# Kernel tuning notes

Hardware: AMD Instinct MI355X
Metric: run time of the kernel (lower is better)

The kernel has to match this reference:

```python
import jax, jax.numpy as jnp
import numpy as np

EMB = 256
HEADS = 16
QKV = 16
SQRT_EMB = 16.0
SQRT_QKV = 4.0
CLIP = 10.0


def setup_inputs() -> dict:
    key = jax.random.key(0)
    ks = jax.random.split(key, 8)
    B, M, J = 64, 128, 512
    s = 1.0 / np.sqrt(EMB)
    return {
        "encoded_machine": jax.random.normal(ks[0], (B, M, EMB), jnp.float32),
        "encoded_jobs": jax.random.normal(ks[1], (B, J, EMB), jnp.float32),
        "ninf_mask": jnp.zeros((B, M, J + 1), jnp.float32),
        "Wq3": jax.random.normal(ks[2], (EMB, HEADS * QKV), jnp.float32) * s,
        "Wk": jax.random.normal(ks[3], (EMB, HEADS * QKV), jnp.float32) * s,
        "Wv": jax.random.normal(ks[4], (EMB, HEADS * QKV), jnp.float32) * s,
        "Wc": jax.random.normal(ks[5], (HEADS * QKV, EMB), jnp.float32) * s,
        "bc": jax.random.normal(ks[6], (EMB,), jnp.float32) * s,
        "skip_emb": jax.random.uniform(ks[7], (1, 1, EMB), jnp.float32),
    }


def _heads(x):
    # (B, N, H*D) -> (B, H, N, D)
    B, N, _ = x.shape
    return x.reshape(B, N, HEADS, QKV).transpose(0, 2, 1, 3)


def reference(encoded_machine, encoded_jobs, ninf_mask, Wq3, Wk, Wv, Wc, bc, skip_emb):
    B, M, _ = encoded_machine.shape
    # prepend learned skip token: (B, T=J+1, E)
    jobs = jnp.concatenate(
        [jnp.broadcast_to(skip_emb, (B, 1, EMB)), encoded_jobs], axis=1)
    T = jobs.shape[1]

    q = _heads(encoded_machine @ Wq3)          # (B,H,M,D)
    k = _heads(jobs @ Wk)                      # (B,H,T,D)
    v = _heads(jobs @ Wv)                      # (B,H,T,D)

    score = jnp.einsum("bhmd,bhtd->bhmt", q, k) / SQRT_QKV
    weights = jax.nn.softmax(score, axis=-1)   # (B,H,M,T)
    out = jnp.einsum("bhmt,bhtd->bhmd", weights, v)
    out_concat = out.transpose(0, 2, 1, 3).reshape(B, M, HEADS * QKV)
    mh = out_concat @ Wc + bc                  # (B,M,E)

    score2 = jnp.einsum("bme,bte->bmt", mh, jobs) / SQRT_EMB
    logits = CLIP * jnp.tanh(score2) + ninf_mask
    probs = jax.nn.softmax(logits.reshape(B, M * T), axis=1)
    return probs
```

## Files before the change

### kernel.cpp

```cpp
#include <hip/hip_runtime.h>
#include <math.h>


#define LDT 68
#define LDB 132
#define TPAD 544
#define NROWS 34816

typedef __attribute__((ext_vector_type(8))) short bf16x8;
typedef __attribute__((ext_vector_type(8))) unsigned short u16x8;
typedef __attribute__((ext_vector_type(4))) float f32x4;
typedef __attribute__((ext_vector_type(4))) unsigned short u16x4;

static __device__ inline unsigned short f2bf(float x) {
  unsigned u = __float_as_uint(x);
  return (unsigned short)((u + 0x7fffu + ((u >> 16) & 1u)) >> 16);
}
static __device__ inline float bf2f(unsigned short h) {
  return __uint_as_float(((unsigned)h) << 16);
}

#define GLD16(gsrc, ldst) \
  __builtin_amdgcn_global_load_lds((const __attribute__((address_space(1))) void*)(gsrc), \
                                   (__attribute__((address_space(3))) void*)(ldst), 16, 0, 0)

__global__ void prep_wt(const float* __restrict__ Wk, const float* __restrict__ Wv,
                        unsigned short* __restrict__ Wh, unsigned short* __restrict__ Wl)
{
  __shared__ unsigned short sh[256], sl[256];
  const int c = blockIdx.x, k = threadIdx.x;
  const float x = (c < 256) ? Wk[k * 256 + c] : Wv[k * 256 + (c - 256)];
  const unsigned short h = f2bf(x);
  sh[k] = h; sl[k] = f2bf(x - bf2f(h));
  __syncthreads();
  if (k < 32)
    *(u16x8*)(Wh + ((size_t)k * 512 + c) * 8) = *(const u16x8*)&sh[k * 8];
  else if (k < 64)
    *(u16x8*)(Wl + ((size_t)(k - 32) * 512 + c) * 8) = *(const u16x8*)&sl[(k - 32) * 8];
}

__global__ __launch_bounds__(256) void prep_jobs(
    const float* __restrict__ jobs, const float* __restrict__ skip,
    unsigned short* __restrict__ Jh, unsigned short* __restrict__ Jl)
{
  const int w = threadIdx.x >> 6, lane = threadIdx.x & 63;
  const int r = blockIdx.x * 64 + lane;
  const int bb = r / TPAD, tt = r - bb * TPAD;
  const bool padr = (tt >= 513);
  const float* src = (tt == 0) ? skip : (jobs + ((size_t)(bb * 512 + tt - 1) << 8));
  #pragma unroll
  for (int i = 0; i < 8; ++i) {
    const int cc = w * 8 + i;
    u16x8 h8 = {}, l8 = {};
    if (!padr) {
      const float4 a = *(const float4*)(src + cc * 8);
      const float4 b = *(const float4*)(src + cc * 8 + 4);
      const float v[8] = {a.x,a.y,a.z,a.w, b.x,b.y,b.z,b.w};
      #pragma unroll
      for (int j = 0; j < 8; ++j) {
        const unsigned short hh = f2bf(v[j]);
        h8[j] = hh;
        l8[j] = f2bf(v[j] - bf2f(hh));
      }
    }
    const size_t o = ((size_t)cc * NROWS + r) * 8;
    *(u16x8*)(Jh + o) = h8;
    *(u16x8*)(Jl + o) = l8;
  }
}

__global__ __launch_bounds__(256) void gemm_kv_mfma(
    const unsigned short* __restrict__ Jh, const unsigned short* __restrict__ Jl,
    const unsigned short* __restrict__ Wh, const unsigned short* __restrict__ Wl,
    unsigned short* __restrict__ Kh, unsigned short* __restrict__ Kl,
    unsigned short* __restrict__ Vth, unsigned short* __restrict__ Vtl)
{
  __shared__ __align__(128) char smem[49152];
  const int tid = threadIdx.x;
  const int lin = blockIdx.x + (blockIdx.y << 2);
  const int virt = (lin & 7) * 272 + (lin >> 3);
  const int bx = virt & 3, by = virt >> 2;
  const int w = __builtin_amdgcn_readfirstlane(tid >> 6);
  const int lane = tid & 63;
  const int wr = (w >> 1) << 5;
  const int wc = (w & 1) << 6;
  const int fm = lane & 15, fq = lane >> 4;

  const unsigned short* sp = (w == 0) ? Jh : (w == 1) ? Jl : (w == 2) ? Wh : Wl;
  const char* srcb = (w < 2)
      ? (const char*)sp + ((size_t)(by * 64) + lane) * 16
      : (const char*)sp + ((size_t)(bx * 128) + lane) * 16;

  auto STAGE = [&](int ks, int bsel) {
    char* buf = smem + bsel * 24576;
    if (w < 2) {
      char* dst = buf + (w ? 4096 : 0);
      #pragma unroll
      for (int j = 0; j < 4; ++j)
        GLD16(srcb + ((size_t)(ks * 4 + j)) * ((size_t)NROWS * 16),
              dst + j * 1024);
    } else {
      char* dst = buf + 8192 + ((w == 3) ? 8192 : 0);
      #pragma unroll
      for (int j = 0; j < 8; ++j) {
        const int fq_ = j >> 1, half = j & 1;
        GLD16(srcb + (((size_t)(ks * 4 + fq_)) * 512 + half * 64) * 16,
              dst + fq_ * 2048 + half * 1024);
      }
    }
  };

  f32x4 acc[2][4] = {};

  STAGE(0, 0);
  STAGE(1, 1);

  #pragma unroll
  for (int ks = 0; ks < 8; ++ks) {
    if (ks < 7) {
      if (w < 2) asm volatile("s_waitcnt vmcnt(4)" ::: "memory");
      else       asm volatile("s_waitcnt vmcnt(8)" ::: "memory");
    } else {
      asm volatile("s_waitcnt vmcnt(0)" ::: "memory");
    }
    __builtin_amdgcn_s_barrier();
    __builtin_amdgcn_sched_barrier(0);

    char* cur = smem + (ks & 1) * 24576;
    bf16x8 afh[2], afl[2], bfh[4], bfl[4];
    #pragma unroll
    for (int i = 0; i < 2; ++i) {
      const int ro = fq * 1024 + (wr + i * 16 + fm) * 16;
      afh[i] = *(const bf16x8*)(cur + ro);
      afl[i] = *(const bf16x8*)(cur + 4096 + ro);
    }
    #pragma unroll
    for (int n = 0; n < 4; ++n) {
      const int co = fq * 2048 + (wc + n * 16 + fm) * 16;
      bfh[n] = *(const bf16x8*)(cur + 8192 + co);
      bfl[n] = *(const bf16x8*)(cur + 16384 + co);
    }
    #pragma unroll
    for (int mi = 0; mi < 2; ++mi)
      #pragma unroll
      for (int ni = 0; ni < 4; ++ni) {
        acc[mi][ni] = __builtin_amdgcn_mfma_f32_16x16x32_bf16(afh[mi], bfl[ni], acc[mi][ni], 0, 0, 0);
        acc[mi][ni] = __builtin_amdgcn_mfma_f32_16x16x32_bf16(afl[mi], bfh[ni], acc[mi][ni], 0, 0, 0);
        acc[mi][ni] = __builtin_amdgcn_mfma_f32_16x16x32_bf16(afh[mi], bfh[ni], acc[mi][ni], 0, 0, 0);
      }

    __builtin_amdgcn_s_barrier();
    if (ks + 2 < 8) STAGE(ks + 2, ks & 1);
  }

  const int cb = ((bx & 1) << 7) + wc;
  if (bx < 2) {
    #pragma unroll
    for (int mi = 0; mi < 2; ++mi) {
      #pragma unroll
      for (int r = 0; r < 4; ++r) {
        const int row = by * 64 + wr + mi * 16 + fq * 4 + r;
        const size_t rb = (size_t)row << 8;
        #pragma unroll
        for (int ni = 0; ni < 4; ++ni) {
          const int cc = cb + ni * 16 + fm;
          const float x = acc[mi][ni][r];
          const unsigned short hh = f2bf(x);
          Kh[rb + cc] = hh;
          Kl[rb + cc] = f2bf(x - bf2f(hh));
        }
      }
    }
  } else {
    #pragma unroll
    for (int mi = 0; mi < 2; ++mi) {
      const int row0 = by * 64 + wr + mi * 16 + fq * 4;
      const int bb = row0 / TPAD;
      const int tt0 = row0 - bb * TPAD;
      #pragma unroll
      for (int ni = 0; ni < 4; ++ni) {
        const int cc = cb + ni * 16 + fm;
        const size_t vb = ((size_t)(bb * 256 + cc)) * TPAD + tt0;
        u16x4 vh, vl;
        #pragma unroll
        for (int r = 0; r < 4; ++r) {
          const float x = acc[mi][ni][r];
          const unsigned short hh = f2bf(x);
          vh[r] = hh;
          vl[r] = f2bf(x - bf2f(hh));
        }
        *(u16x4*)(Vth + vb) = vh;
        *(u16x4*)(Vtl + vb) = vl;
      }
    }
  }
}

template<int MODE>
__global__ __launch_bounds__(256) void gemm_wide(
    const float* __restrict__ A, const float* __restrict__ W,
    const float* __restrict__ bias, float* __restrict__ C1,
    unsigned short* __restrict__ Ch, unsigned short* __restrict__ Cl)
{
  __shared__ float As[16 * LDT];
  __shared__ float Bs[16 * LDB];
  const int tid = threadIdx.x;
  const int bx = blockIdx.x, by = blockIdx.y;
  const int col0 = bx * 128;

  const int a_row = tid >> 2;
  const int a_k4  = (tid & 3) << 2;
  const float* arow = A + ((size_t)(by * 64 + a_row) << 8);

  const int b_k  = tid >> 4;
  const int b_c8 = (tid & 15) << 3;

  const int tr = tid >> 4, tc = tid & 15;
  float acc[4][8] = {};

  for (int k0 = 0; k0 < 256; k0 += 16) {
    const float4 av  = *(const float4*)(arow + k0 + a_k4);
    const float4 bv0 = *(const float4*)(W + ((size_t)(k0 + b_k) << 8) + col0 + b_c8);
    const float4 bv1 = *(const float4*)(W + ((size_t)(k0 + b_k) << 8) + col0 + b_c8 + 4);
    __syncthreads();
    As[(a_k4 + 0) * LDT + a_row] = av.x;
    As[(a_k4 + 1) * LDT + a_row] = av.y;
    As[(a_k4 + 2) * LDT + a_row] = av.z;
    As[(a_k4 + 3) * LDT + a_row] = av.w;
    *(float4*)&Bs[b_k * LDB + b_c8]     = bv0;
    *(float4*)&Bs[b_k * LDB + b_c8 + 4] = bv1;
    __syncthreads();
    #pragma unroll
    for (int k = 0; k < 16; ++k) {
      const float4 a  = *(const float4*)&As[k * LDT + (tr << 2)];
      const float4 b0 = *(const float4*)&Bs[k * LDB + (tc << 3)];
      const float4 b1 = *(const float4*)&Bs[k * LDB + (tc << 3) + 4];
      const float aa[4] = {a.x, a.y, a.z, a.w};
      #pragma unroll
      for (int i = 0; i < 4; ++i) {
        acc[i][0] = fmaf(aa[i], b0.x, acc[i][0]);
        acc[i][1] = fmaf(aa[i], b0.y, acc[i][1]);
        acc[i][2] = fmaf(aa[i], b0.z, acc[i][2]);
        acc[i][3] = fmaf(aa[i], b0.w, acc[i][3]);
        acc[i][4] = fmaf(aa[i], b1.x, acc[i][4]);
        acc[i][5] = fmaf(aa[i], b1.y, acc[i][5]);
        acc[i][6] = fmaf(aa[i], b1.z, acc[i][6]);
        acc[i][7] = fmaf(aa[i], b1.w, acc[i][7]);
      }
    }
  }

  const int oc = col0 + (tc << 3);
  float4 bsa = make_float4(0.f,0.f,0.f,0.f), bsb = make_float4(0.f,0.f,0.f,0.f);
  if (bias) { bsa = *(const float4*)(bias + oc); bsb = *(const float4*)(bias + oc + 4); }
  const float bb[8] = {bsa.x,bsa.y,bsa.z,bsa.w, bsb.x,bsb.y,bsb.z,bsb.w};
  #pragma unroll
  for (int i = 0; i < 4; ++i) {
    const int row = by * 64 + (tr << 2) + i;
    if (MODE == 0) {
      float* crow = C1 + ((size_t)row << 8) + oc;
      float4 o0, o1;
      o0.x = acc[i][0]+bb[0]; o0.y = acc[i][1]+bb[1]; o0.z = acc[i][2]+bb[2]; o0.w = acc[i][3]+bb[3];
      o1.x = acc[i][4]+bb[4]; o1.y = acc[i][5]+bb[5]; o1.z = acc[i][6]+bb[6]; o1.w = acc[i][7]+bb[7];
      *(float4*)crow = o0; *(float4*)(crow + 4) = o1;
    } else {
      u16x8 h8, l8;
      #pragma unroll
      for (int j = 0; j < 8; ++j) {
        const float x = acc[i][j] + bb[j];
        const unsigned short hh = f2bf(x);
        h8[j] = hh;
        l8[j] = f2bf(x - bf2f(hh));
      }
      const size_t o = ((size_t)(oc >> 3) * 8192 + row) * 8;
      *(u16x8*)(Ch + o) = h8;
      *(u16x8*)(Cl + o) = l8;
    }
  }
}

__global__ __launch_bounds__(256, 4) void attn_mfma(
    const float* __restrict__ Q,
    const unsigned short* __restrict__ Kh, const unsigned short* __restrict__ Kl,
    const unsigned short* __restrict__ Vth, const unsigned short* __restrict__ Vtl,
    float* __restrict__ OC)
{
  const int h = blockIdx.x, b = blockIdx.y;
  const int tid = threadIdx.x;
  const int lane = tid & 63;
  const int w = __builtin_amdgcn_readfirstlane(tid >> 6);
  const int g = lane >> 4, fm = lane & 15;
  const int mh = (w & 2) << 5;
  const int th = w & 1;
  const int send = th ? 17 : 9;
  int s = th ? 9 : 0;

  __shared__ float red[2 * 64 * 21];

  const int col = h * 16;
  const int dbase = (g & 1) << 3;

  bf16x8 Bq1[4], Bq2[4];
  #pragma unroll
  for (int mt = 0; mt < 4; ++mt) {
    const float* qp = Q + ((size_t)(b * 128 + mh + mt * 16 + fm) << 8) + col + dbase;
    const float4 q0 = *(const float4*)qp;
    const float4 q1 = *(const float4*)(qp + 4);
    const float qv[8] = {q0.x,q0.y,q0.z,q0.w, q1.x,q1.y,q1.z,q1.w};
    #pragma unroll
    for (int j = 0; j < 8; ++j) {
      const float x = qv[j] * 0.25f;
      const unsigned short hh = f2bf(x);
      Bq1[mt][j] = (short)hh;
      Bq2[mt][j] = (short)((g < 2) ? f2bf(x - bf2f(hh)) : (unsigned short)0);
    }
  }

  f32x4 oT[4] = {};
  float lsum[4] = {0.f, 0.f, 0.f, 0.f};

  const int rA = ((fm & 12) << 1) + (fm & 3);
  const unsigned short* kpl = ((g < 2) ? Kh : Kl)
      + ((((size_t)b * TPAD) + rA) << 8) + col + dbase;
  const unsigned short* vhp = Vth + ((size_t)(b * 256 + col + fm)) * TPAD + (g << 3);
  const unsigned short* vlp = Vtl + ((size_t)(b * 256 + col + fm)) * TPAD + (g << 3);

  for (; s < send; ++s) {
    const int t0 = s << 5;
    const bf16x8 KA = *(const bf16x8*)(kpl + ((size_t)t0 << 8));
    const bf16x8 KB = *(const bf16x8*)(kpl + ((size_t)(t0 + 4) << 8));
    const bf16x8 Vh = *(const bf16x8*)(vhp + t0);
    const bf16x8 Vl = *(const bf16x8*)(vlp + t0);

    #pragma unroll
    for (int mt = 0; mt < 4; ++mt) {
      f32x4 sA = {}, sB = {};
      sA = __builtin_amdgcn_mfma_f32_16x16x32_bf16(KA, Bq1[mt], sA, 0, 0, 0);
      sA = __builtin_amdgcn_mfma_f32_16x16x32_bf16(KA, Bq2[mt], sA, 0, 0, 0);
      sB = __builtin_amdgcn_mfma_f32_16x16x32_bf16(KB, Bq1[mt], sB, 0, 0, 0);
      sB = __builtin_amdgcn_mfma_f32_16x16x32_bf16(KB, Bq2[mt], sB, 0, 0, 0);
      float p[8];
      p[0] = __expf(sA[0]); p[1] = __expf(sA[1]); p[2] = __expf(sA[2]); p[3] = __expf(sA[3]);
      p[4] = __expf(sB[0]); p[5] = __expf(sB[1]); p[6] = __expf(sB[2]); p[7] = __expf(sB[3]);
      lsum[mt] += ((p[0] + p[1]) + (p[2] + p[3])) + ((p[4] + p[5]) + (p[6] + p[7]));
      bf16x8 Ph, Pl;
      #pragma unroll
      for (int jp = 0; jp < 4; ++jp) {
        const unsigned u0 = __float_as_uint(p[2*jp]);
        const unsigned u1 = __float_as_uint(p[2*jp+1]);
        ((unsigned*)&Ph)[jp] = __builtin_amdgcn_perm(u1, u0, 0x07060302u);
        const float r0 = p[2*jp]   - __uint_as_float(u0 & 0xffff0000u);
        const float r1 = p[2*jp+1] - __uint_as_float(u1 & 0xffff0000u);
        unsigned t0_ = __float_as_uint(r0); t0_ += 0x7fffu + ((t0_ >> 16) & 1u);
        unsigned t1_ = __float_as_uint(r1); t1_ += 0x7fffu + ((t1_ >> 16) & 1u);
        ((unsigned*)&Pl)[jp] = __builtin_amdgcn_perm(t1_, t0_, 0x07060302u);
      }
      oT[mt] = __builtin_amdgcn_mfma_f32_16x16x32_bf16(Vh, Ph, oT[mt], 0, 0, 0);
      oT[mt] = __builtin_amdgcn_mfma_f32_16x16x32_bf16(Vh, Pl, oT[mt], 0, 0, 0);
      oT[mt] = __builtin_amdgcn_mfma_f32_16x16x32_bf16(Vl, Ph, oT[mt], 0, 0, 0);
    }
  }

  float* slot = red + ((w >> 1) * 1344);
  const int base = lane * 21;
  if (th) {
    #pragma unroll
    for (int mt = 0; mt < 4; ++mt) {
      slot[base + 4 * mt + 0] = oT[mt][0];
      slot[base + 4 * mt + 1] = oT[mt][1];
      slot[base + 4 * mt + 2] = oT[mt][2];
      slot[base + 4 * mt + 3] = oT[mt][3];
      slot[base + 16 + mt]    = lsum[mt];
    }
  }
  __syncthreads();
  if (!th) {
    #pragma unroll
    for (int mt = 0; mt < 4; ++mt) {
      oT[mt][0] += slot[base + 4 * mt + 0];
      oT[mt][1] += slot[base + 4 * mt + 1];
      oT[mt][2] += slot[base + 4 * mt + 2];
      oT[mt][3] += slot[base + 4 * mt + 3];
      float v = lsum[mt] + slot[base + 16 + mt];
      v += __shfl_xor(v, 16);
      v += __shfl_xor(v, 32);
      const float inv = 1.f / (v - 31.f);
      float4 o;
      o.x = oT[mt][0] * inv; o.y = oT[mt][1] * inv;
      o.z = oT[mt][2] * inv; o.w = oT[mt][3] * inv;
      *(float4*)(OC + ((size_t)(b * 128 + mh + mt * 16 + fm) << 8) + col + (g << 2)) = o;
    }
  }
}

__global__ __launch_bounds__(256) void logits_mfma(
    const unsigned short* __restrict__ Mh, const unsigned short* __restrict__ Ml,
    const unsigned short* __restrict__ Jh, const unsigned short* __restrict__ Jl,
    const float* __restrict__ mask,
    float* __restrict__ out, float* __restrict__ partials)
{
  __shared__ __align__(128) char smem[49152];
  __shared__ float red[4];
  const int tid = threadIdx.x;
  const int lin = blockIdx.x + blockIdx.y * 9;
  const int virt = (lin & 7) * 72 + (lin >> 3);
  const int tx = virt % 9;
  const int b  = virt / 9;
  const int w = __builtin_amdgcn_readfirstlane(tid >> 6);
  const int lane = tid & 63;
  const int wr = (w >> 1) << 6;
  const int wtc = (w & 1) << 5;
  const int fm = lane & 15, fq = lane >> 4;

  const unsigned short* sp = (w == 0) ? Mh : (w == 1) ? Ml : (w == 2) ? Jh : Jl;
  int jrow = b * TPAD + tx * 64 + lane;
  if (jrow > NROWS - 1) jrow = NROWS - 1;
  const char* srcb = (w < 2)
      ? (const char*)sp + ((size_t)(b * 128) + lane) * 16
      : (const char*)sp + (size_t)jrow * 16;

  auto STAGE = [&](int ks, int bsel) {
    char* buf = smem + bsel * 24576;
    if (w < 2) {
      char* dst = buf + (w ? 8192 : 0);
      #pragma unroll
      for (int j = 0; j < 8; ++j) {
        const int fq_ = j >> 1, half = j & 1;
        GLD16(srcb + (((size_t)(ks * 4 + fq_)) * 8192 + half * 64) * 16,
              dst + fq_ * 2048 + half * 1024);
      }
    } else {
      char* dst = buf + 16384 + ((w == 3) ? 4096 : 0);
      #pragma unroll
      for (int j = 0; j < 4; ++j)
        GLD16(srcb + ((size_t)(ks * 4 + j)) * ((size_t)NROWS * 16),
              dst + j * 1024);
    }
  };

  f32x4 acc[4][2] = {};

  STAGE(0, 0);
  STAGE(1, 1);

  #pragma unroll
  for (int ks = 0; ks < 8; ++ks) {
    if (ks < 7) {
      if (w < 2) asm volatile("s_waitcnt vmcnt(8)" ::: "memory");
      else       asm volatile("s_waitcnt vmcnt(4)" ::: "memory");
    } else {
      asm volatile("s_waitcnt vmcnt(0)" ::: "memory");
    }
    __builtin_amdgcn_s_barrier();
    __builtin_amdgcn_sched_barrier(0);

    char* cur = smem + (ks & 1) * 24576;
    bf16x8 afh[4], afl[4], bfh[2], bfl[2];
    #pragma unroll
    for (int i = 0; i < 4; ++i) {
      const int ro = fq * 2048 + (wr + i * 16 + fm) * 16;
      afh[i] = *(const bf16x8*)(cur + ro);
      afl[i] = *(const bf16x8*)(cur + 8192 + ro);
    }
    #pragma unroll
    for (int n = 0; n < 2; ++n) {
      const int co = fq * 1024 + (wtc + n * 16 + fm) * 16;
      bfh[n] = *(const bf16x8*)(cur + 16384 + co);
      bfl[n] = *(const bf16x8*)(cur + 20480 + co);
    }
    #pragma unroll
    for (int mi = 0; mi < 4; ++mi)
      #pragma unroll
      for (int ni = 0; ni < 2; ++ni) {
        acc[mi][ni] = __builtin_amdgcn_mfma_f32_16x16x32_bf16(afh[mi], bfl[ni], acc[mi][ni], 0, 0, 0);
        acc[mi][ni] = __builtin_amdgcn_mfma_f32_16x16x32_bf16(afl[mi], bfh[ni], acc[mi][ni], 0, 0, 0);
        acc[mi][ni] = __builtin_amdgcn_mfma_f32_16x16x32_bf16(afh[mi], bfh[ni], acc[mi][ni], 0, 0, 0);
      }

    __builtin_amdgcn_s_barrier();
    if (ks + 2 < 8) STAGE(ks + 2, ks & 1);
  }

  float lsum = 0.f;
  #pragma unroll
  for (int mi = 0; mi < 4; ++mi) {
    #pragma unroll
    for (int r = 0; r < 4; ++r) {
      const int m = wr + mi * 16 + fq * 4 + r;
      #pragma unroll
      for (int ni = 0; ni < 2; ++ni) {
        const int t = tx * 64 + wtc + ni * 16 + fm;
        if (t < 513) {
          const float e2 = __expf(acc[mi][ni][r] * 0.125f);
          const float e  = __expf(mask[((size_t)(b * 128 + m)) * 513 + t]
                                  - 20.f / (e2 + 1.f));
          out[(size_t)b * 65664 + (size_t)m * 513 + t] = e;
          lsum += e;
        }
      }
    }
  }
  #pragma unroll
  for (int off = 32; off; off >>= 1) lsum += __shfl_xor(lsum, off);
  if (lane == 0) red[w] = lsum;
  __syncthreads();
  if (tid == 0)
    partials[b * 9 + tx] = (red[0] + red[1]) + (red[2] + red[3]);
}

__global__ __launch_bounds__(256) void sm_norm(float* __restrict__ out,
                                               const float* __restrict__ partials)
{
  const int i4 = blockIdx.x * 256 + threadIdx.x;
  if (i4 < 1050624) {
    const int b = i4 / 16416;
    float s = 0.f;
    #pragma unroll
    for (int i = 0; i < 9; ++i) s += partials[b * 9 + i];
    const float inv = 1.f / s;
    float4 v = ((float4*)out)[i4];
    v.x *= inv; v.y *= inv; v.z *= inv; v.w *= inv;
    ((float4*)out)[i4] = v;
  }
}

extern "C" void kernel_launch(void* const* d_in, const int* in_sizes, int n_in,
                              void* d_out, int out_size, void* d_ws, size_t ws_size,
                              hipStream_t stream)
{
  const float* machine = (const float*)d_in[0];
  const float* jobs    = (const float*)d_in[1];
  const float* mask    = (const float*)d_in[2];
  const float* Wq      = (const float*)d_in[3];
  const float* Wk      = (const float*)d_in[4];
  const float* Wv      = (const float*)d_in[5];
  const float* Wc      = (const float*)d_in[6];
  const float* bc      = (const float*)d_in[7];
  const float* skip    = (const float*)d_in[8];

  float* ws       = (float*)d_ws;
  unsigned short* JhP = (unsigned short*)ws;
  unsigned short* JlP = JhP + 8912896;
  unsigned short* KhP = (unsigned short*)(ws + 8912896);
  unsigned short* KlP = KhP + 8912896;
  unsigned short* VthP = (unsigned short*)(ws + 17825792);
  unsigned short* VtlP = VthP + 8912896;
  unsigned short* WhP = (unsigned short*)(ws + 26738688);
  unsigned short* WlP = WhP + 131072;
  unsigned short* MhP = (unsigned short*)(ws + 8912896);
  unsigned short* MlP = MhP + 2097152;
  float* partials = ws + 26738688;
  float* out      = (float*)d_out;
  float* Qw       = out;
  float* OC       = out + 2097152;

  prep_wt<<<512, 256, 0, stream>>>(Wk, Wv, WhP, WlP);
  prep_jobs<<<544, 256, 0, stream>>>(jobs, skip, JhP, JlP);
  gemm_kv_mfma<<<dim3(4, 544), 256, 0, stream>>>(
      JhP, JlP, WhP, WlP, KhP, KlP, VthP, VtlP);
  gemm_wide<0><<<dim3(2, 128), 256, 0, stream>>>(
      machine, Wq, nullptr, Qw, nullptr, nullptr);
  attn_mfma<<<dim3(16, 64), 256, 0, stream>>>(Qw, KhP, KlP, VthP, VtlP, OC);
  gemm_wide<1><<<dim3(2, 128), 256, 0, stream>>>(
      OC, Wc, bc, nullptr, MhP, MlP);
  logits_mfma<<<dim3(9, 64), 256, 0, stream>>>(
      MhP, MlP, JhP, JlP, mask, out, partials);
  sm_norm<<<4104, 256, 0, stream>>>(out, partials);
}
```

Before: 290.2 us.

## Move Q and output projections to split-bf16 MFMA and fuse bf16 handoff

Replaces the two fp32 FMA projection GEMMs (machine@Wq and attention_out@Wc) with a new MFMA kernel that uses hi/lo bf16 splitting, matching the K/V GEMM. All four weight matrices are now pre-split in one prep kernel, and a new prep kernel splits the machine embeddings. Attention now reads pre-scaled, pre-split Q and writes its output directly in split bf16 layout, so the per-element float-to-bf16 conversion work in attn moves out of the inner setup. The split-bf16 scheme drops the lo*lo term, which loses a little precision. The epilogue also uses scalar 16-bit stores and adds an extra launch.

```diff
diff --git a/kernel.cpp b/kernel.cpp
--- a/kernel.cpp
+++ b/kernel.cpp
@@ -2,8 +2,6 @@
 #include <math.h>
 
 
-#define LDT 68
-#define LDB 132
 #define TPAD 544
 #define NROWS 34816
 
@@ -24,19 +22,21 @@
   __builtin_amdgcn_global_load_lds((const __attribute__((address_space(1))) void*)(gsrc), \
                                    (__attribute__((address_space(3))) void*)(ldst), 16, 0, 0)
 
-__global__ void prep_wt(const float* __restrict__ Wk, const float* __restrict__ Wv,
+__global__ void prep_wt(const float* __restrict__ Wq, const float* __restrict__ Wk,
+                        const float* __restrict__ Wv, const float* __restrict__ Wc,
                         unsigned short* __restrict__ Wh, unsigned short* __restrict__ Wl)
 {
   __shared__ unsigned short sh[256], sl[256];
   const int c = blockIdx.x, k = threadIdx.x;
-  const float x = (c < 256) ? Wk[k * 256 + c] : Wv[k * 256 + (c - 256)];
+  const float* Ws = (c < 256) ? Wq : (c < 512) ? Wk : (c < 768) ? Wv : Wc;
+  const float x = Ws[k * 256 + (c & 255)];
   const unsigned short h = f2bf(x);
   sh[k] = h; sl[k] = f2bf(x - bf2f(h));
   __syncthreads();
   if (k < 32)
-    *(u16x8*)(Wh + ((size_t)k * 512 + c) * 8) = *(const u16x8*)&sh[k * 8];
+    *(u16x8*)(Wh + ((size_t)k * 1024 + c) * 8) = *(const u16x8*)&sh[k * 8];
   else if (k < 64)
-    *(u16x8*)(Wl + ((size_t)(k - 32) * 512 + c) * 8) = *(const u16x8*)&sl[(k - 32) * 8];
+    *(u16x8*)(Wl + ((size_t)(k - 32) * 1024 + c) * 8) = *(const u16x8*)&sl[(k - 32) * 8];
 }
 
 __global__ __launch_bounds__(256) void prep_jobs(
@@ -66,6 +66,32 @@
     const size_t o = ((size_t)cc * NROWS + r) * 8;
     *(u16x8*)(Jh + o) = h8;
     *(u16x8*)(Jl + o) = l8;
+  }
+}
+
+__global__ __launch_bounds__(256) void prep_mach(
+    const float* __restrict__ A,
+    unsigned short* __restrict__ Mh, unsigned short* __restrict__ Ml)
+{
+  const int w = threadIdx.x >> 6, lane = threadIdx.x & 63;
+  const int r = blockIdx.x * 64 + lane;
+  const float* src = A + ((size_t)r << 8);
+  #pragma unroll
+  for (int i = 0; i < 8; ++i) {
+    const int cc = w * 8 + i;
+    const float4 a = *(const float4*)(src + cc * 8);
+    const float4 b = *(const float4*)(src + cc * 8 + 4);
+    const float v[8] = {a.x,a.y,a.z,a.w, b.x,b.y,b.z,b.w};
+    u16x8 h8, l8;
+    #pragma unroll
+    for (int j = 0; j < 8; ++j) {
+      const unsigned short hh = f2bf(v[j]);
+      h8[j] = hh;
+      l8[j] = f2bf(v[j] - bf2f(hh));
+    }
+    const size_t o = ((size_t)cc * 8192 + r) * 8;
+    *(u16x8*)(Mh + o) = h8;
+    *(u16x8*)(Ml + o) = l8;
   }
 }
 
@@ -89,7 +115,7 @@
   const unsigned short* sp = (w == 0) ? Jh : (w == 1) ? Jl : (w == 2) ? Wh : Wl;
   const char* srcb = (w < 2)
       ? (const char*)sp + ((size_t)(by * 64) + lane) * 16
-      : (const char*)sp + ((size_t)(bx * 128) + lane) * 16;
+      : (const char*)sp + ((size_t)(256 + bx * 128) + lane) * 16;
 
   auto STAGE = [&](int ks, int bsel) {
     char* buf = smem + bsel * 24576;
@@ -104,7 +130,7 @@
       #pragma unroll
       for (int j = 0; j < 8; ++j) {
         const int fq_ = j >> 1, half = j & 1;
-        GLD16(srcb + (((size_t)(ks * 4 + fq_)) * 512 + half * 64) * 16,
+        GLD16(srcb + (((size_t)(ks * 4 + fq_)) * 1024 + half * 64) * 16,
               dst + fq_ * 2048 + half * 1024);
       }
     }
@@ -196,94 +222,95 @@
   }
 }
 
-template<int MODE>
-__global__ __launch_bounds__(256) void gemm_wide(
-    const float* __restrict__ A, const float* __restrict__ W,
-    const float* __restrict__ bias, float* __restrict__ C1,
+__global__ __launch_bounds__(256) void proj_mfma(
+    const unsigned short* __restrict__ Ah_, const unsigned short* __restrict__ Al_,
+    const unsigned short* __restrict__ Wh_, const unsigned short* __restrict__ Wl_,
+    const int cbase, const float scale, const float* __restrict__ bias,
     unsigned short* __restrict__ Ch, unsigned short* __restrict__ Cl)
 {
-  __shared__ float As[16 * LDT];
-  __shared__ float Bs[16 * LDB];
+  __shared__ __align__(128) char smem[32768];
   const int tid = threadIdx.x;
-  const int bx = blockIdx.x, by = blockIdx.y;
-  const int col0 = bx * 128;
-
-  const int a_row = tid >> 2;
-  const int a_k4  = (tid & 3) << 2;
-  const float* arow = A + ((size_t)(by * 64 + a_row) << 8);
-
-  const int b_k  = tid >> 4;
-  const int b_c8 = (tid & 15) << 3;
-
-  const int tr = tid >> 4, tc = tid & 15;
-  float acc[4][8] = {};
-
-  for (int k0 = 0; k0 < 256; k0 += 16) {
-    const float4 av  = *(const float4*)(arow + k0 + a_k4);
-    const float4 bv0 = *(const float4*)(W + ((size_t)(k0 + b_k) << 8) + col0 + b_c8);
-    const float4 bv1 = *(const float4*)(W + ((size_t)(k0 + b_k) << 8) + col0 + b_c8 + 4);
-    __syncthreads();
-    As[(a_k4 + 0) * LDT + a_row] = av.x;
-    As[(a_k4 + 1) * LDT + a_row] = av.y;
-    As[(a_k4 + 2) * LDT + a_row] = av.z;
-    As[(a_k4 + 3) * LDT + a_row] = av.w;
-    *(float4*)&Bs[b_k * LDB + b_c8]     = bv0;
-    *(float4*)&Bs[b_k * LDB + b_c8 + 4] = bv1;
-    __syncthreads();
-    #pragma unroll
-    for (int k = 0; k < 16; ++k) {
-      const float4 a  = *(const float4*)&As[k * LDT + (tr << 2)];
-      const float4 b0 = *(const float4*)&Bs[k * LDB + (tc << 3)];
-      const float4 b1 = *(const float4*)&Bs[k * LDB + (tc << 3) + 4];
-      const float aa[4] = {a.x, a.y, a.z, a.w};
-      #pragma unroll
-      for (int i = 0; i < 4; ++i) {
-        acc[i][0] = fmaf(aa[i], b0.x, acc[i][0]);
-        acc[i][1] = fmaf(aa[i], b0.y, acc[i][1]);
-        acc[i][2] = fmaf(aa[i], b0.z, acc[i][2]);
-        acc[i][3] = fmaf(aa[i], b0.w, acc[i][3]);
-        acc[i][4] = fmaf(aa[i], b1.x, acc[i][4]);
-        acc[i][5] = fmaf(aa[i], b1.y, acc[i][5]);
-        acc[i][6] = fmaf(aa[i], b1.z, acc[i][6]);
-        acc[i][7] = fmaf(aa[i], b1.w, acc[i][7]);
-      }
-    }
-  }
-
-  const int oc = col0 + (tc << 3);
-  float4 bsa = make_float4(0.f,0.f,0.f,0.f), bsb = make_float4(0.f,0.f,0.f,0.f);
-  if (bias) { bsa = *(const float4*)(bias + oc); bsb = *(const float4*)(bias + oc + 4); }
-  const float bb[8] = {bsa.x,bsa.y,bsa.z,bsa.w, bsb.x,bsb.y,bsb.z,bsb.w};
-  #pragma unroll
-  for (int i = 0; i < 4; ++i) {
-    const int row = by * 64 + (tr << 2) + i;
-    if (MODE == 0) {
-      float* crow = C1 + ((size_t)row << 8) + oc;
-      float4 o0, o1;
-      o0.x = acc[i][0]+bb[0]; o0.y = acc[i][1]+bb[1]; o0.z = acc[i][2]+bb[2]; o0.w = acc[i][3]+bb[3];
-      o1.x = acc[i][4]+bb[4]; o1.y = acc[i][5]+bb[5]; o1.z = acc[i][6]+bb[6]; o1.w = acc[i][7]+bb[7];
-      *(float4*)crow = o0; *(float4*)(crow + 4) = o1;
-    } else {
-      u16x8 h8, l8;
-      #pragma unroll
-      for (int j = 0; j < 8; ++j) {
-        const float x = acc[i][j] + bb[j];
+  const int lin = blockIdx.x + (blockIdx.y << 2);
+  const int virt = (lin & 7) * 64 + (lin >> 3);
+  const int bx = virt & 3, by = virt >> 2;
+  const int w = __builtin_amdgcn_readfirstlane(tid >> 6);
+  const int lane = tid & 63;
+  const int wr = (w >> 1) << 5, wc = (w & 1) << 5;
+  const int fm = lane & 15, fq = lane >> 4;
+
+  const unsigned short* sp = (w == 0) ? Ah_ : (w == 1) ? Al_ : (w == 2) ? Wh_ : Wl_;
+  const size_t rstride = (w < 2) ? (size_t)8192 : (size_t)1024;
+  const size_t base = (w < 2) ? (size_t)(by * 64) : (size_t)(cbase + bx * 64);
+  const char* srcb = (const char*)sp + (base + lane) * 16;
+
+  auto STAGE = [&](int ks, int bsel) {
+    char* dst = smem + bsel * 16384 + w * 4096;
+    #pragma unroll
+    for (int j = 0; j < 4; ++j)
+      GLD16(srcb + ((size_t)(ks * 4 + j)) * rstride * 16, dst + j * 1024);
+  };
+
+  f32x4 acc[2][2] = {};
+
+  STAGE(0, 0);
+  STAGE(1, 1);
+
+  #pragma unroll
+  for (int ks = 0; ks < 8; ++ks) {
+    if (ks < 7) asm volatile("s_waitcnt vmcnt(4)" ::: "memory");
+    else        asm volatile("s_waitcnt vmcnt(0)" ::: "memory");
+    __builtin_amdgcn_s_barrier();
+    __builtin_amdgcn_sched_barrier(0);
+
+    char* cur = smem + (ks & 1) * 16384;
+    bf16x8 afh[2], afl[2], bfh[2], bfl[2];
+    #pragma unroll
+    for (int i = 0; i < 2; ++i) {
+      const int ro = fq * 1024 + (wr + i * 16 + fm) * 16;
+      const int co = fq * 1024 + (wc + i * 16 + fm) * 16;
+      afh[i] = *(const bf16x8*)(cur + ro);
+      afl[i] = *(const bf16x8*)(cur + 4096 + ro);
+      bfh[i] = *(const bf16x8*)(cur + 8192 + co);
+      bfl[i] = *(const bf16x8*)(cur + 12288 + co);
+    }
+    #pragma unroll
+    for (int mi = 0; mi < 2; ++mi)
+      #pragma unroll
+      for (int ni = 0; ni < 2; ++ni) {
+        acc[mi][ni] = __builtin_amdgcn_mfma_f32_16x16x32_bf16(afh[mi], bfl[ni], acc[mi][ni], 0, 0, 0);
+        acc[mi][ni] = __builtin_amdgcn_mfma_f32_16x16x32_bf16(afl[mi], bfh[ni], acc[mi][ni], 0, 0, 0);
+        acc[mi][ni] = __builtin_amdgcn_mfma_f32_16x16x32_bf16(afh[mi], bfh[ni], acc[mi][ni], 0, 0, 0);
+      }
+
+    __builtin_amdgcn_s_barrier();
+    if (ks + 2 < 8) STAGE(ks + 2, ks & 1);
+  }
+
+  const int colb = bx * 64 + wc;
+  #pragma unroll
+  for (int mi = 0; mi < 2; ++mi) {
+    #pragma unroll
+    for (int r = 0; r < 4; ++r) {
+      const int row = by * 64 + wr + mi * 16 + fq * 4 + r;
+      #pragma unroll
+      for (int ni = 0; ni < 2; ++ni) {
+        const int oc = colb + ni * 16 + fm;
+        float x = acc[mi][ni][r] * scale;
+        if (bias) x += bias[oc];
         const unsigned short hh = f2bf(x);
-        h8[j] = hh;
-        l8[j] = f2bf(x - bf2f(hh));
-      }
-      const size_t o = ((size_t)(oc >> 3) * 8192 + row) * 8;
-      *(u16x8*)(Ch + o) = h8;
-      *(u16x8*)(Cl + o) = l8;
+        const size_t o = ((size_t)(oc >> 3) * 8192 + row) * 8 + (oc & 7);
+        Ch[o] = hh;
+        Cl[o] = f2bf(x - bf2f(hh));
+      }
     }
   }
 }
 
 __global__ __launch_bounds__(256, 4) void attn_mfma(
-    const float* __restrict__ Q,
+    const unsigned short* __restrict__ Qh, const unsigned short* __restrict__ Ql,
     const unsigned short* __restrict__ Kh, const unsigned short* __restrict__ Kl,
     const unsigned short* __restrict__ Vth, const unsigned short* __restrict__ Vtl,
-    float* __restrict__ OC)
+    unsigned short* __restrict__ Och, unsigned short* __restrict__ Ocl)
 {
   const int h = blockIdx.x, b = blockIdx.y;
   const int tid = threadIdx.x;
@@ -298,28 +325,22 @@
   __shared__ float red[2 * 64 * 21];
 
   const int col = h * 16;
-  const int dbase = (g & 1) << 3;
 
   bf16x8 Bq1[4], Bq2[4];
+  const bf16x8 zf = {};
   #pragma unroll
   for (int mt = 0; mt < 4; ++mt) {
-    const float* qp = Q + ((size_t)(b * 128 + mh + mt * 16 + fm) << 8) + col + dbase;
-    const float4 q0 = *(const float4*)qp;
-    const float4 q1 = *(const float4*)(qp + 4);
-    const float qv[8] = {q0.x,q0.y,q0.z,q0.w, q1.x,q1.y,q1.z,q1.w};
-    #pragma unroll
-    for (int j = 0; j < 8; ++j) {
-      const float x = qv[j] * 0.25f;
-      const unsigned short hh = f2bf(x);
-      Bq1[mt][j] = (short)hh;
-      Bq2[mt][j] = (short)((g < 2) ? f2bf(x - bf2f(hh)) : (unsigned short)0);
-    }
+    const size_t qo = ((size_t)(h * 2 + (g & 1)) * 8192
+                      + (b * 128 + mh + mt * 16 + fm)) * 8;
+    Bq1[mt] = *(const bf16x8*)(Qh + qo);
+    Bq2[mt] = (g < 2) ? *(const bf16x8*)(Ql + qo) : zf;
   }
 
   f32x4 oT[4] = {};
   float lsum[4] = {0.f, 0.f, 0.f, 0.f};
 
   const int rA = ((fm & 12) << 1) + (fm & 3);
+  const int dbase = (g & 1) << 3;
   const unsigned short* kpl = ((g < 2) ? Kh : Kl)
       + ((((size_t)b * TPAD) + rA) << 8) + col + dbase;
   const unsigned short* vhp = Vth + ((size_t)(b * 256 + col + fm)) * TPAD + (g << 3);
@@ -385,10 +406,18 @@
       v += __shfl_xor(v, 16);
       v += __shfl_xor(v, 32);
       const float inv = 1.f / (v - 31.f);
-      float4 o;
-      o.x = oT[mt][0] * inv; o.y = oT[mt][1] * inv;
-      o.z = oT[mt][2] * inv; o.w = oT[mt][3] * inv;
-      *(float4*)(OC + ((size_t)(b * 128 + mh + mt * 16 + fm) << 8) + col + (g << 2)) = o;
+      const int row = b * 128 + mh + mt * 16 + fm;
+      const size_t oo = ((size_t)(h * 2 + (g >> 1)) * 8192 + row) * 8 + ((g & 1) << 2);
+      u16x4 oh, ol;
+      #pragma unroll
+      for (int r = 0; r < 4; ++r) {
+        const float x = oT[mt][r] * inv;
+        const unsigned short hh = f2bf(x);
+        oh[r] = hh;
+        ol[r] = f2bf(x - bf2f(hh));
+      }
+      *(u16x4*)(Och + oo) = oh;
+      *(u16x4*)(Ocl + oo) = ol;
     }
   }
 }
@@ -545,24 +574,30 @@
   unsigned short* KlP = KhP + 8912896;
   unsigned short* VthP = (unsigned short*)(ws + 17825792);
   unsigned short* VtlP = VthP + 8912896;
-  unsigned short* WhP = (unsigned short*)(ws + 26738688);
-  unsigned short* WlP = WhP + 131072;
-  unsigned short* MhP = (unsigned short*)(ws + 8912896);
-  unsigned short* MlP = MhP + 2097152;
-  float* partials = ws + 26738688;
+  unsigned short* WahP = (unsigned short*)(ws + 26738688);
+  unsigned short* WalP = WahP + 262144;
+  unsigned short* MchP = (unsigned short*)(ws + 27000832);
+  unsigned short* MclP = MchP + 2097152;
+  unsigned short* MhP  = (unsigned short*)(ws + 8912896);
+  unsigned short* MlP  = MhP + 2097152;
+  float* partials = ws + 29097984;
   float* out      = (float*)d_out;
-  float* Qw       = out;
-  float* OC       = out + 2097152;
-
-  prep_wt<<<512, 256, 0, stream>>>(Wk, Wv, WhP, WlP);
+  unsigned short* QhP  = (unsigned short*)out;
+  unsigned short* QlP  = QhP + 2097152;
+  unsigned short* OchP = QlP + 2097152;
+  unsigned short* OclP = OchP + 2097152;
+
+  prep_wt<<<1024, 256, 0, stream>>>(Wq, Wk, Wv, Wc, WahP, WalP);
   prep_jobs<<<544, 256, 0, stream>>>(jobs, skip, JhP, JlP);
+  prep_mach<<<128, 256, 0, stream>>>(machine, MchP, MclP);
   gemm_kv_mfma<<<dim3(4, 544), 256, 0, stream>>>(
-      JhP, JlP, WhP, WlP, KhP, KlP, VthP, VtlP);
-  gemm_wide<0><<<dim3(2, 128), 256, 0, stream>>>(
-      machine, Wq, nullptr, Qw, nullptr, nullptr);
-  attn_mfma<<<dim3(16, 64), 256, 0, stream>>>(Qw, KhP, KlP, VthP, VtlP, OC);
-  gemm_wide<1><<<dim3(2, 128), 256, 0, stream>>>(
-      OC, Wc, bc, nullptr, MhP, MlP);
+      JhP, JlP, WahP, WalP, KhP, KlP, VthP, VtlP);
+  proj_mfma<<<dim3(4, 128), 256, 0, stream>>>(
+      MchP, MclP, WahP, WalP, 0, 0.25f, nullptr, QhP, QlP);
+  attn_mfma<<<dim3(16, 64), 256, 0, stream>>>(
+      QhP, QlP, KhP, KlP, VthP, VtlP, OchP, OclP);
+  proj_mfma<<<dim3(4, 128), 256, 0, stream>>>(
+      OchP, OclP, WahP, WalP, 768, 1.0f, bc, MhP, MlP);
   logits_mfma<<<dim3(9, 64), 256, 0, stream>>>(
       MhP, MlP, JhP, JlP, mask, out, partials);
   sm_norm<<<4104, 256, 0, stream>>>(out, partials);
```

Result: faster. 242.9 us (-16.3%).
